# Performance work log

Measured on AMD Instinct MI355X. Metric: run time of the kernel, lower is better.

## Reference

```python
import jax, jax.numpy as jnp
import numpy as np

B, N, C = 4, 2048, 1024
H = 16
D = C // H  # head_dim = 64
NEG = -1e9


def setup_inputs() -> dict:
    key = jax.random.key(0)
    k1, k2, k3, k4 = jax.random.split(key, 4)
    x = jax.random.normal(k1, (B, N, C), dtype=jnp.float32)
    # additive causal mask [N, N]: 0 on/below diagonal, -1e9 above
    causal = jnp.tril(jnp.ones((N, N), dtype=bool))
    attn_mask = jnp.where(causal, 0.0, NEG).astype(jnp.float32)
    # params: qkv Dense (no bias, qkv_bias=False), proj Dense (with bias)
    W_qkv = jax.random.normal(k2, (C, 3 * C), dtype=jnp.float32) / np.sqrt(C)
    W_proj = jax.random.normal(k3, (C, C), dtype=jnp.float32) / np.sqrt(C)
    b_proj = jnp.zeros((C,), dtype=jnp.float32)
    return {"x": x, "attn_mask": attn_mask, "W_qkv": W_qkv,
            "W_proj": W_proj, "b_proj": b_proj}


def reference(x, attn_mask, W_qkv, W_proj, b_proj):
    b, n, c = x.shape
    # qkv projection -> [B, N, 3, H, D] -> q,k,v each [B, H, N, D]
    qkv = (x @ W_qkv).reshape(b, n, 3, H, D)
    qkv = jnp.transpose(qkv, (2, 0, 3, 1, 4))
    q, k, v = qkv[0], qkv[1], qkv[2]
    # unfused attention: full [B, H, N, N] score matrix
    scores = jnp.einsum('bhnd,bhmd->bhnm', q, k) / np.sqrt(D).astype(jnp.float32)
    scores = scores + attn_mask  # broadcast [N, N] over batch/heads
    attn_w = jax.nn.softmax(scores.astype(jnp.float32), axis=-1).astype(scores.dtype)
    out = jnp.einsum('bhnm,bhmd->bhnd', attn_w, v)
    out = jnp.transpose(out, (0, 2, 1, 3)).reshape(b, n, c)
    return out @ W_proj + b_proj
```

## Files before the change

kernel.cpp:

```cpp
#include <hip/hip_runtime.h>
#include <stdint.h>


typedef short s16x8 __attribute__((ext_vector_type(8)));
typedef float f32x4 __attribute__((ext_vector_type(4)));
typedef int i32x2 __attribute__((ext_vector_type(2)));
typedef unsigned int u32;

__device__ __forceinline__ uint16_t f2bf(float f) {
  union { float f; uint32_t u; } v; v.f = f;
  uint32_t r = v.u + 0x7fffu + ((v.u >> 16) & 1u);
  return (uint16_t)(r >> 16);
}

__device__ __forceinline__ u32 cvt_pk_bf16(float lo, float hi) {
  u32 r;
  asm("v_cvt_pk_bf16_f32 %0, %1, %2" : "=v"(r) : "v"(lo), "v"(hi));
  return r;
}

__device__ __forceinline__ s16x8 pack4(u32 w0, u32 w1, u32 w2, u32 w3) {
  union { u32 u[4]; s16x8 v; } t;
  t.u[0] = w0; t.u[1] = w1; t.u[2] = w2; t.u[3] = w3;
  return t.v;
}

#define GLOAD_LDS16(g, l)                                            \
  __builtin_amdgcn_global_load_lds(                                  \
      (const __attribute__((address_space(1))) void*)(g),            \
      (__attribute__((address_space(3))) void*)(l), 16, 0, 0)

__device__ __forceinline__ void transpose32_body(
    const float* __restrict__ src, uint16_t* __restrict__ dst,
    int R, int C, int bx32, int by32, uint16_t (*tile)[33], int tid) {
  const int tx = tid & 31, ty = tid >> 5;
#pragma unroll
  for (int i = 0; i < 32; i += 8)
    tile[ty + i][tx] = f2bf(src[(size_t)(by32 + ty + i) * C + bx32 + tx]);
  __syncthreads();
#pragma unroll
  for (int i = 0; i < 32; i += 8)
    dst[(size_t)(bx32 + ty + i) * R + by32 + tx] = tile[tx][ty + i];
}

__global__ __launch_bounds__(256) void prep_kernel(
    const float* __restrict__ x, uint16_t* __restrict__ xbf,
    const float* __restrict__ Wqkv, uint16_t* __restrict__ wqkvT,
    const float* __restrict__ Wproj, uint16_t* __restrict__ wprojT) {
  __shared__ uint16_t tile[32][33];
  const int bid = blockIdx.x;
  if (bid < 4096) {
    const int i = bid * 256 + threadIdx.x;
    const f32x4 a = ((const f32x4*)x)[2 * i];
    const f32x4 b = ((const f32x4*)x)[2 * i + 1];
    s16x8 r;
    r[0] = (short)f2bf(a[0]); r[1] = (short)f2bf(a[1]);
    r[2] = (short)f2bf(a[2]); r[3] = (short)f2bf(a[3]);
    r[4] = (short)f2bf(b[0]); r[5] = (short)f2bf(b[1]);
    r[6] = (short)f2bf(b[2]); r[7] = (short)f2bf(b[3]);
    ((s16x8*)xbf)[i] = r;
  } else if (bid < 4096 + 3072) {
    const int t = bid - 4096;
    transpose32_body(Wqkv, wqkvT, 1024, 3072, (t % 96) * 32, (t / 96) * 32,
                     tile, threadIdx.x);
  } else {
    const int t = bid - 7168;
    transpose32_body(Wproj, wprojT, 1024, 1024, (t & 31) * 32, (t >> 5) * 32,
                     tile, threadIdx.x);
  }
}

__global__ __launch_bounds__(256) void vtrans_kernel(
    const uint16_t* __restrict__ src, uint16_t* __restrict__ dst) {
  const int bh = blockIdx.y >> 1, dhalf = blockIdx.y & 1;
  const int n0 = blockIdx.x * 32, d0 = dhalf * 32;
  const uint16_t* sb = src + (size_t)bh * 131072;
  uint16_t* db = dst + (size_t)bh * 131072;
  __shared__ uint16_t tile[32][33];
  const int tx = threadIdx.x & 31, ty = threadIdx.x >> 5;
#pragma unroll
  for (int i = 0; i < 32; i += 8)
    tile[ty + i][tx] = sb[(size_t)(n0 + ty + i) * 64 + d0 + tx];
  __syncthreads();
#pragma unroll
  for (int i = 0; i < 32; i += 8)
    db[(size_t)(d0 + ty + i) * 2048 + n0 + tx] = tile[tx][ty + i];
}

template <bool ROUTE>
__global__ __launch_bounds__(256) void gemm_bt_kernel(
    const uint16_t* __restrict__ A, const uint16_t* __restrict__ Bt,
    float* __restrict__ Cout,
    uint16_t* __restrict__ rq, uint16_t* __restrict__ rk, uint16_t* __restrict__ rv,
    const float* __restrict__ bias, int M, int N, int K) {
  __shared__ uint16_t sA[128 * 32];
  __shared__ uint16_t sB[128 * 32];
  const int tid = threadIdx.x;
  const int lane = tid & 63, w = tid >> 6;
  const int l15 = lane & 15, quad = lane >> 4;
  const int row0 = blockIdx.y * 128, col0 = blockIdx.x * 128;
  const int wm = (w >> 1) * 64, wn = (w & 1) * 64;

  f32x4 acc[4][4];
#pragma unroll
  for (int i = 0; i < 4; ++i)
#pragma unroll
    for (int j = 0; j < 4; ++j)
#pragma unroll
      for (int e = 0; e < 4; ++e) acc[i][j][e] = 0.0f;

  for (int k0 = 0; k0 < K; k0 += 32) {
    __syncthreads();
#pragma unroll
    for (int i = 0; i < 2; ++i) {
      const int cbase = i * 256 + w * 64;
      const int c = cbase + lane;
      const int r = c >> 2, kc = (c & 3) * 8;
      GLOAD_LDS16(A + (size_t)(row0 + r) * K + k0 + kc, sA + cbase * 8);
      GLOAD_LDS16(Bt + (size_t)(col0 + r) * K + k0 + kc, sB + cbase * 8);
    }
    __syncthreads();

    s16x8 aF[4], bF[4];
#pragma unroll
    for (int mt = 0; mt < 4; ++mt)
      aF[mt] = *(const s16x8*)(sA + (wm + mt * 16 + l15) * 32 + quad * 8);
#pragma unroll
    for (int nt = 0; nt < 4; ++nt)
      bF[nt] = *(const s16x8*)(sB + (wn + nt * 16 + l15) * 32 + quad * 8);
#pragma unroll
    for (int mt = 0; mt < 4; ++mt)
#pragma unroll
      for (int nt = 0; nt < 4; ++nt)
        acc[mt][nt] = __builtin_amdgcn_mfma_f32_16x16x32_bf16(aF[mt], bF[nt], acc[mt][nt], 0, 0, 0);
  }

  if (ROUTE) {
    const int which = col0 >> 10;
    uint16_t* dst = (which == 0) ? rq : ((which == 1) ? rk : rv);
    const float qs = (which == 0) ? 0.18033688011112042f : 1.0f;
#pragma unroll
    for (int mt = 0; mt < 4; ++mt) {
#pragma unroll
      for (int nt = 0; nt < 4; ++nt) {
        const int colg0 = col0 + wn + nt * 16;
        const int h = (colg0 >> 6) & 15, d0 = colg0 & 63;
#pragma unroll
        for (int i = 0; i < 4; ++i) {
          const int rowg = row0 + wm + mt * 16 + quad * 4 + i;
          const int bh = ((rowg >> 11) << 4) + h, n = rowg & 2047;
          dst[(size_t)bh * 131072 + (size_t)n * 64 + d0 + l15] = f2bf(acc[mt][nt][i] * qs);
        }
      }
    }
  } else {
#pragma unroll
    for (int mt = 0; mt < 4; ++mt) {
#pragma unroll
      for (int nt = 0; nt < 4; ++nt) {
        const int colg = col0 + wn + nt * 16 + l15;
        const float bv = bias[colg];
#pragma unroll
        for (int i = 0; i < 4; ++i) {
          const int rowg = row0 + wm + mt * 16 + quad * 4 + i;
          Cout[(size_t)rowg * N + colg] = acc[mt][nt][i] + bv;
        }
      }
    }
  }
}

__global__ __launch_bounds__(256) void attn_kernel(
    const uint16_t* __restrict__ q_ws, const uint16_t* __restrict__ k_ws,
    const uint16_t* __restrict__ vt_ws, uint16_t* __restrict__ out) {
  const int p = blockIdx.x;
  const int bh = blockIdx.y;
  const int b = bh >> 4, h = bh & 15;
  const int q0L = p * 64, q0H = (31 - p) * 64;
  const int tid = threadIdx.x;
  const int lane = tid & 63, w = tid >> 6;
  const int l15 = lane & 15, quad = lane >> 4;
  const bool qeven = (quad & 1) == 0;

  const uint16_t* qb = q_ws + (size_t)bh * 131072;
  const uint16_t* kb = k_ws + (size_t)bh * 131072;
  const uint16_t* vtb = vt_ws + (size_t)bh * 131072;

  __shared__ uint16_t sK[2][64 * 72];
  __shared__ uint16_t sV[2][64 * 72];

  const int qrowL = q0L + w * 16 + l15;
  const int qrowH = q0H + w * 16 + l15;
  const s16x8 aQL0 = *(const s16x8*)(qb + (size_t)qrowL * 64 + quad * 8);
  const s16x8 aQL1 = *(const s16x8*)(qb + (size_t)qrowL * 64 + 32 + quad * 8);
  const s16x8 aQH0 = *(const s16x8*)(qb + (size_t)qrowH * 64 + quad * 8);
  const s16x8 aQH1 = *(const s16x8*)(qb + (size_t)qrowH * 64 + 32 + quad * 8);

  f32x4 oL[4], oH[4], laccL, laccH;
#pragma unroll
  for (int e = 0; e < 4; ++e) { laccL[e] = 0.0f; laccH[e] = 0.0f; }
#pragma unroll
  for (int i = 0; i < 4; ++i)
#pragma unroll
    for (int e = 0; e < 4; ++e) { oL[i][e] = 0.0f; oH[i][e] = 0.0f; }

  s16x8 bOnes;
#pragma unroll
  for (int j = 0; j < 8; ++j) bOnes[j] = (short)0x3F80;

  const int vr = tid >> 2, dc = (tid & 3) * 16;
  s16x8 rk0 = *(const s16x8*)(kb + (size_t)vr * 64 + dc);
  s16x8 rk1 = *(const s16x8*)(kb + (size_t)vr * 64 + dc + 8);
  s16x8 rv0 = *(const s16x8*)(vtb + (size_t)vr * 2048 + dc);
  s16x8 rv1 = *(const s16x8*)(vtb + (size_t)vr * 2048 + dc + 8);

  const int qrel = w * 16 + l15;

  auto qkt = [&](const s16x8& a0, const s16x8& a1, const uint16_t* sKb,
                 f32x4 (&s)[4]) {
#pragma unroll
    for (int nt = 0; nt < 4; ++nt) {
      f32x4 z;
#pragma unroll
      for (int e = 0; e < 4; ++e) z[e] = 0.0f;
      const s16x8 bK0 = *(const s16x8*)(sKb + (nt * 16 + l15) * 72 + quad * 8);
      const s16x8 bK1 = *(const s16x8*)(sKb + (nt * 16 + l15) * 72 + 32 + quad * 8);
      s[nt] = __builtin_amdgcn_mfma_f32_16x16x32_bf16(bK0, a0, z, 0, 0, 0);
      s[nt] = __builtin_amdgcn_mfma_f32_16x16x32_bf16(bK1, a1, s[nt], 0, 0, 0);
    }
  };

  auto finish = [&](const f32x4 (&s)[4], bool diag, f32x4* o, f32x4& lacc,
                    const uint16_t* sVb) {
#pragma unroll
    for (int kk = 0; kk < 2; ++kk) {
      u32 w0, w1, w2, w3;
#pragma unroll
      for (int t2 = 0; t2 < 2; ++t2) {
        const f32x4& sv = s[2 * kk + t2];
        float pp[4];
        if (diag) {
          const int nt = 2 * kk + t2;
#pragma unroll
          for (int i = 0; i < 4; ++i) {
            const int kv = nt * 16 + quad * 4 + i;
            pp[i] = (kv > qrel) ? 0.0f : __builtin_amdgcn_exp2f(sv[i]);
          }
        } else {
#pragma unroll
          for (int i = 0; i < 4; ++i) pp[i] = __builtin_amdgcn_exp2f(sv[i]);
        }
        const u32 lo = cvt_pk_bf16(pp[0], pp[1]);
        const u32 hi = cvt_pk_bf16(pp[2], pp[3]);
        if (t2 == 0) { w0 = lo; w1 = hi; } else { w2 = lo; w3 = hi; }
      }
      const i32x2 r0 = __builtin_amdgcn_permlane32_swap((int)w0, (int)w2, false, false);
      const i32x2 r1 = __builtin_amdgcn_permlane32_swap((int)w1, (int)w3, false, false);
      const u32 A0 = (u32)r0[0], B0 = (u32)r0[1];
      const u32 A1 = (u32)r1[0], B1 = (u32)r1[1];
      const u32 u0 = qeven ? B0 : A0;
      const u32 u1 = qeven ? B1 : A1;
      const u32 x0 = __shfl_xor(u0, 16);
      const u32 x1 = __shfl_xor(u1, 16);
      const s16x8 aP = pack4(qeven ? A0 : x0, qeven ? A1 : x1,
                             qeven ? x0 : B0, qeven ? x1 : B1);
      lacc = __builtin_amdgcn_mfma_f32_16x16x32_bf16(aP, bOnes, lacc, 0, 0, 0);
#pragma unroll
      for (int dblk = 0; dblk < 4; ++dblk) {
        const s16x8 bV = *(const s16x8*)(sVb + (dblk * 16 + l15) * 72 + kk * 32 + quad * 8);
        o[dblk] = __builtin_amdgcn_mfma_f32_16x16x32_bf16(aP, bV, o[dblk], 0, 0, 0);
      }
    }
  };

  const int TH = q0H >> 6;
  const int TL = q0L >> 6;
  f32x4 sHp[4];

  for (int t = 0; t <= TH; ++t) {
    const int buf = t & 1;
    uint16_t* sKb = sK[buf];
    uint16_t* sVb = sV[buf];
    *(s16x8*)(sKb + vr * 72 + dc) = rk0;
    *(s16x8*)(sKb + vr * 72 + dc + 8) = rk1;
    *(s16x8*)(sVb + vr * 72 + dc) = rv0;
    *(s16x8*)(sVb + vr * 72 + dc + 8) = rv1;
    if (t < TH) {
      const int kvn = (t + 1) << 6;
      rk0 = *(const s16x8*)(kb + (size_t)(kvn + vr) * 64 + dc);
      rk1 = *(const s16x8*)(kb + (size_t)(kvn + vr) * 64 + dc + 8);
      rv0 = *(const s16x8*)(vtb + (size_t)vr * 2048 + kvn + dc);
      rv1 = *(const s16x8*)(vtb + (size_t)vr * 2048 + kvn + dc + 8);
    }
    if (t >= 1) finish(sHp, false, oH, laccH, sV[buf ^ 1]);
    __syncthreads();
    qkt(aQH0, aQH1, sKb, sHp);
    if (t <= TL) {
      f32x4 sLt[4];
      qkt(aQL0, aQL1, sKb, sLt);
      finish(sLt, t == TL, oL, laccL, sVb);
    }
  }
  finish(sHp, true, oH, laccH, sV[TH & 1]);

  const size_t obase = (size_t)b * 2048 * 1024 + (size_t)h * 64;
  auto epi = [&](f32x4* o, const f32x4& lacc, int q0) {
#pragma unroll
    for (int i = 0; i < 4; ++i) {
      const float invi = 1.0f / lacc[i];
      const int row = q0 + w * 16 + quad * 4 + i;
#pragma unroll
      for (int dblk = 0; dblk < 4; ++dblk)
        out[obase + (size_t)row * 1024 + dblk * 16 + l15] = f2bf(o[dblk][i] * invi);
    }
  };
  epi(oH, laccH, q0H);
  epi(oL, laccL, q0L);
}

extern "C" void kernel_launch(void* const* d_in, const int* in_sizes, int n_in,
                              void* d_out, int out_size, void* d_ws, size_t ws_size,
                              hipStream_t stream) {
  (void)in_sizes; (void)n_in; (void)out_size; (void)ws_size;
  const float* x     = (const float*)d_in[0];
  const float* Wqkv  = (const float*)d_in[2];
  const float* Wproj = (const float*)d_in[3];
  const float* bproj = (const float*)d_in[4];
  float* outp = (float*)d_out;

  uint16_t* ws      = (uint16_t*)d_ws;
  uint16_t* q_ws    = ws;
  uint16_t* k_ws    = ws + (size_t)8388608;
  uint16_t* v_ws    = ws + (size_t)16777216;
  uint16_t* attn_ws = ws + (size_t)16777216;
  uint16_t* wqkvT   = ws + (size_t)25165824;
  uint16_t* wprojT  = ws + (size_t)28311552;
  uint16_t* xbf     = (uint16_t*)d_out;
  uint16_t* vt_ws   = (uint16_t*)d_out;

  prep_kernel<<<8192, 256, 0, stream>>>(x, xbf, Wqkv, wqkvT, Wproj, wprojT);
  gemm_bt_kernel<true><<<dim3(24, 64), 256, 0, stream>>>(
      xbf, wqkvT, nullptr, q_ws, k_ws, v_ws, nullptr, 8192, 3072, 1024);
  vtrans_kernel<<<dim3(64, 128), 256, 0, stream>>>(v_ws, vt_ws);
  attn_kernel<<<dim3(16, 64), 256, 0, stream>>>(q_ws, k_ws, vt_ws, attn_ws);
  gemm_bt_kernel<false><<<dim3(8, 64), 256, 0, stream>>>(
      attn_ws, wprojT, outp, nullptr, nullptr, nullptr, bproj, 8192, 1024, 1024);
}
```

Before: 276.6 us.

## Add dedicated double-buffered 256x256 QKV GEMM kernel with swizzled LDS

```diff
diff --git a/kernel.cpp b/kernel.cpp
--- a/kernel.cpp
+++ b/kernel.cpp
@@ -87,12 +87,122 @@
     db[(size_t)(d0 + ty + i) * 2048 + n0 + tx] = tile[tx][ty + i];
 }
 
-template <bool ROUTE>
+__global__ __launch_bounds__(512, 2) void gemm1_kernel(
+    const uint16_t* __restrict__ A, const uint16_t* __restrict__ Bt,
+    uint16_t* __restrict__ rq, uint16_t* __restrict__ rk,
+    uint16_t* __restrict__ rv) {
+  constexpr int K = 1024;
+  constexpr int NT = 16;
+  __shared__ uint16_t sA[2][256 * 64];
+  __shared__ uint16_t sB[2][256 * 64];
+  const int tid = threadIdx.x;
+  const int lane = tid & 63, w = tid >> 6;
+  const int l15 = lane & 15, quad = lane >> 4;
+  const int row0 = blockIdx.y * 256, col0 = blockIdx.x * 256;
+  const int wm = (w >> 2) * 128, wn = (w & 3) * 64;
+
+  const int rA = lane >> 3;
+  const int cXe = ((lane & 7) ^ rA) * 8;
+  const int sgBase = w * 2048;
+
+  const int sx = l15 & 7;
+  const int ok0 = (quad ^ sx) * 8;
+  const int ok1 = ((quad + 4) ^ sx) * 8;
+
+  f32x4 acc[8][4];
+#pragma unroll
+  for (int i = 0; i < 8; ++i)
+#pragma unroll
+    for (int j = 0; j < 4; ++j)
+#pragma unroll
+      for (int e = 0; e < 4; ++e) acc[i][j][e] = 0.0f;
+
+  auto stageA = [&](uint16_t* dst, int kt) {
+#pragma unroll
+    for (int j = 0; j < 4; ++j)
+      GLOAD_LDS16(A + (size_t)(row0 + w * 32 + j * 8 + rA) * K + kt * 64 + cXe,
+                  dst + sgBase + j * 512);
+  };
+  auto stageB = [&](uint16_t* dst, int kt) {
+#pragma unroll
+    for (int j = 0; j < 4; ++j)
+      GLOAD_LDS16(Bt + (size_t)(col0 + w * 32 + j * 8 + rA) * K + kt * 64 + cXe,
+                  dst + sgBase + j * 512);
+  };
+
+  stageA(sA[0], 0);
+  stageB(sB[0], 0);
+
+  int cur = 0;
+  for (int t = 0; t < NT; ++t) {
+    const uint16_t* Ab = sA[cur];
+    const uint16_t* Bb = sB[cur];
+    uint16_t* An = sA[cur ^ 1];
+    uint16_t* Bn = sB[cur ^ 1];
+    const bool haveNext = (t < NT - 1);
+    s16x8 bF[4][2];
+#pragma unroll
+    for (int p = 0; p < 4; ++p) {
+      if (p == 0) {
+        if (haveNext) {
+          stageA(An, t + 1);
+          asm volatile("s_waitcnt vmcnt(4)" ::: "memory");
+        } else {
+          asm volatile("s_waitcnt vmcnt(0)" ::: "memory");
+        }
+        asm volatile("s_barrier" ::: "memory");
+#pragma unroll
+        for (int nt = 0; nt < 4; ++nt) {
+          bF[nt][0] = *(const s16x8*)(Bb + (wn + nt * 16 + l15) * 64 + ok0);
+          bF[nt][1] = *(const s16x8*)(Bb + (wn + nt * 16 + l15) * 64 + ok1);
+        }
+      }
+      if (p == 1 && haveNext) stageB(Bn, t + 1);
+      const int r0 = wm + p * 32 + l15;
+      const s16x8 a00 = *(const s16x8*)(Ab + r0 * 64 + ok0);
+      const s16x8 a01 = *(const s16x8*)(Ab + r0 * 64 + ok1);
+      const s16x8 a10 = *(const s16x8*)(Ab + (r0 + 16) * 64 + ok0);
+      const s16x8 a11 = *(const s16x8*)(Ab + (r0 + 16) * 64 + ok1);
+      __builtin_amdgcn_s_setprio(1);
+#pragma unroll
+      for (int nt = 0; nt < 4; ++nt) {
+        acc[2 * p][nt] =
+            __builtin_amdgcn_mfma_f32_16x16x32_bf16(a00, bF[nt][0], acc[2 * p][nt], 0, 0, 0);
+        acc[2 * p][nt] =
+            __builtin_amdgcn_mfma_f32_16x16x32_bf16(a01, bF[nt][1], acc[2 * p][nt], 0, 0, 0);
+        acc[2 * p + 1][nt] =
+            __builtin_amdgcn_mfma_f32_16x16x32_bf16(a10, bF[nt][0], acc[2 * p + 1][nt], 0, 0, 0);
+        acc[2 * p + 1][nt] =
+            __builtin_amdgcn_mfma_f32_16x16x32_bf16(a11, bF[nt][1], acc[2 * p + 1][nt], 0, 0, 0);
+      }
+      __builtin_amdgcn_s_setprio(0);
+      asm volatile("s_barrier" ::: "memory");
+    }
+    cur ^= 1;
+  }
+
+  const int which = col0 >> 10;
+  uint16_t* dst = (which == 0) ? rq : ((which == 1) ? rk : rv);
+  const float qs = (which == 0) ? 0.18033688011112042f : 1.0f;
+#pragma unroll
+  for (int mt = 0; mt < 8; ++mt) {
+#pragma unroll
+    for (int nt = 0; nt < 4; ++nt) {
+      const int colg0 = col0 + wn + nt * 16;
+      const int h = (colg0 >> 6) & 15, d0 = colg0 & 63;
+#pragma unroll
+      for (int i = 0; i < 4; ++i) {
+        const int rowg = row0 + wm + mt * 16 + quad * 4 + i;
+        const int bh = ((rowg >> 11) << 4) + h, n = rowg & 2047;
+        dst[(size_t)bh * 131072 + (size_t)n * 64 + d0 + l15] = f2bf(acc[mt][nt][i] * qs);
+      }
+    }
+  }
+}
+
 __global__ __launch_bounds__(256) void gemm_bt_kernel(
     const uint16_t* __restrict__ A, const uint16_t* __restrict__ Bt,
-    float* __restrict__ Cout,
-    uint16_t* __restrict__ rq, uint16_t* __restrict__ rk, uint16_t* __restrict__ rv,
-    const float* __restrict__ bias, int M, int N, int K) {
+    float* __restrict__ Cout, const float* __restrict__ bias, int M, int N, int K) {
   __shared__ uint16_t sA[128 * 32];
   __shared__ uint16_t sB[128 * 32];
   const int tid = threadIdx.x;
@@ -135,36 +245,16 @@
         acc[mt][nt] = __builtin_amdgcn_mfma_f32_16x16x32_bf16(aF[mt], bF[nt], acc[mt][nt], 0, 0, 0);
   }
 
-  if (ROUTE) {
-    const int which = col0 >> 10;
-    uint16_t* dst = (which == 0) ? rq : ((which == 1) ? rk : rv);
-    const float qs = (which == 0) ? 0.18033688011112042f : 1.0f;
-#pragma unroll
-    for (int mt = 0; mt < 4; ++mt) {
-#pragma unroll
-      for (int nt = 0; nt < 4; ++nt) {
-        const int colg0 = col0 + wn + nt * 16;
-        const int h = (colg0 >> 6) & 15, d0 = colg0 & 63;
-#pragma unroll
-        for (int i = 0; i < 4; ++i) {
-          const int rowg = row0 + wm + mt * 16 + quad * 4 + i;
-          const int bh = ((rowg >> 11) << 4) + h, n = rowg & 2047;
-          dst[(size_t)bh * 131072 + (size_t)n * 64 + d0 + l15] = f2bf(acc[mt][nt][i] * qs);
-        }
-      }
-    }
-  } else {
-#pragma unroll
-    for (int mt = 0; mt < 4; ++mt) {
-#pragma unroll
-      for (int nt = 0; nt < 4; ++nt) {
-        const int colg = col0 + wn + nt * 16 + l15;
-        const float bv = bias[colg];
-#pragma unroll
-        for (int i = 0; i < 4; ++i) {
-          const int rowg = row0 + wm + mt * 16 + quad * 4 + i;
-          Cout[(size_t)rowg * N + colg] = acc[mt][nt][i] + bv;
-        }
+#pragma unroll
+  for (int mt = 0; mt < 4; ++mt) {
+#pragma unroll
+    for (int nt = 0; nt < 4; ++nt) {
+      const int colg = col0 + wn + nt * 16 + l15;
+      const float bv = bias[colg];
+#pragma unroll
+      for (int i = 0; i < 4; ++i) {
+        const int rowg = row0 + wm + mt * 16 + quad * 4 + i;
+        Cout[(size_t)rowg * N + colg] = acc[mt][nt][i] + bv;
       }
     }
   }
@@ -339,10 +429,9 @@
   uint16_t* vt_ws   = (uint16_t*)d_out;
 
   prep_kernel<<<8192, 256, 0, stream>>>(x, xbf, Wqkv, wqkvT, Wproj, wprojT);
-  gemm_bt_kernel<true><<<dim3(24, 64), 256, 0, stream>>>(
-      xbf, wqkvT, nullptr, q_ws, k_ws, v_ws, nullptr, 8192, 3072, 1024);
+  gemm1_kernel<<<dim3(12, 32), 512, 0, stream>>>(xbf, wqkvT, q_ws, k_ws, v_ws);
   vtrans_kernel<<<dim3(64, 128), 256, 0, stream>>>(v_ws, vt_ws);
   attn_kernel<<<dim3(16, 64), 256, 0, stream>>>(q_ws, k_ws, vt_ws, attn_ws);
-  gemm_bt_kernel<false><<<dim3(8, 64), 256, 0, stream>>>(
-      attn_ws, wprojT, outp, nullptr, nullptr, nullptr, bproj, 8192, 1024, 1024);
-}
+  gemm_bt_kernel<<<dim3(8, 64), 256, 0, stream>>>(
+      attn_ws, wprojT, outp, bproj, 8192, 1024, 1024);
+}
```

Result: slower. 292.4 us (+5.7%).

## Double GEMM K-tile with XOR-swizzled LDS; drop P-operand permlane shuffles in attention

Applied to the files above, without the earlier changes.

```diff
diff --git a/kernel.cpp b/kernel.cpp
--- a/kernel.cpp
+++ b/kernel.cpp
@@ -3,8 +3,8 @@
 
 
 typedef short s16x8 __attribute__((ext_vector_type(8)));
+typedef short s16x4 __attribute__((ext_vector_type(4)));
 typedef float f32x4 __attribute__((ext_vector_type(4)));
-typedef int i32x2 __attribute__((ext_vector_type(2)));
 typedef unsigned int u32;
 
 __device__ __forceinline__ uint16_t f2bf(float f) {
@@ -22,6 +22,12 @@
 __device__ __forceinline__ s16x8 pack4(u32 w0, u32 w1, u32 w2, u32 w3) {
   union { u32 u[4]; s16x8 v; } t;
   t.u[0] = w0; t.u[1] = w1; t.u[2] = w2; t.u[3] = w3;
+  return t.v;
+}
+
+__device__ __forceinline__ s16x8 pack2h(s16x4 a, s16x4 b) {
+  union { s16x4 h[2]; s16x8 v; } t;
+  t.h[0] = a; t.h[1] = b;
   return t.v;
 }
 
@@ -93,8 +99,8 @@
     float* __restrict__ Cout,
     uint16_t* __restrict__ rq, uint16_t* __restrict__ rk, uint16_t* __restrict__ rv,
     const float* __restrict__ bias, int M, int N, int K) {
-  __shared__ uint16_t sA[128 * 32];
-  __shared__ uint16_t sB[128 * 32];
+  __shared__ uint16_t sA[128 * 64];
+  __shared__ uint16_t sB[128 * 64];
   const int tid = threadIdx.x;
   const int lane = tid & 63, w = tid >> 6;
   const int l15 = lane & 15, quad = lane >> 4;
@@ -109,30 +115,37 @@
 #pragma unroll
       for (int e = 0; e < 4; ++e) acc[i][j][e] = 0.0f;
 
-  for (int k0 = 0; k0 < K; k0 += 32) {
+  const int sx = l15 & 7;
+  const int ok[2] = {((0 * 4 + quad) ^ sx) * 8, ((1 * 4 + quad) ^ sx) * 8};
+
+  for (int k0 = 0; k0 < K; k0 += 64) {
     __syncthreads();
 #pragma unroll
-    for (int i = 0; i < 2; ++i) {
+    for (int i = 0; i < 4; ++i) {
       const int cbase = i * 256 + w * 64;
       const int c = cbase + lane;
-      const int r = c >> 2, kc = (c & 3) * 8;
+      const int r = c >> 3;
+      const int kc = ((c & 7) ^ (r & 7)) * 8;
       GLOAD_LDS16(A + (size_t)(row0 + r) * K + k0 + kc, sA + cbase * 8);
       GLOAD_LDS16(Bt + (size_t)(col0 + r) * K + k0 + kc, sB + cbase * 8);
     }
     __syncthreads();
 
-    s16x8 aF[4], bF[4];
-#pragma unroll
-    for (int mt = 0; mt < 4; ++mt)
-      aF[mt] = *(const s16x8*)(sA + (wm + mt * 16 + l15) * 32 + quad * 8);
-#pragma unroll
-    for (int nt = 0; nt < 4; ++nt)
-      bF[nt] = *(const s16x8*)(sB + (wn + nt * 16 + l15) * 32 + quad * 8);
-#pragma unroll
-    for (int mt = 0; mt < 4; ++mt)
+#pragma unroll
+    for (int kk = 0; kk < 2; ++kk) {
+      s16x8 aF[4], bF[4];
+#pragma unroll
+      for (int mt = 0; mt < 4; ++mt)
+        aF[mt] = *(const s16x8*)(sA + (wm + mt * 16 + l15) * 64 + ok[kk]);
 #pragma unroll
       for (int nt = 0; nt < 4; ++nt)
-        acc[mt][nt] = __builtin_amdgcn_mfma_f32_16x16x32_bf16(aF[mt], bF[nt], acc[mt][nt], 0, 0, 0);
+        bF[nt] = *(const s16x8*)(sB + (wn + nt * 16 + l15) * 64 + ok[kk]);
+#pragma unroll
+      for (int mt = 0; mt < 4; ++mt)
+#pragma unroll
+        for (int nt = 0; nt < 4; ++nt)
+          acc[mt][nt] = __builtin_amdgcn_mfma_f32_16x16x32_bf16(aF[mt], bF[nt], acc[mt][nt], 0, 0, 0);
+    }
   }
 
   if (ROUTE) {
@@ -180,7 +193,6 @@
   const int tid = threadIdx.x;
   const int lane = tid & 63, w = tid >> 6;
   const int l15 = lane & 15, quad = lane >> 4;
-  const bool qeven = (quad & 1) == 0;
 
   const uint16_t* qb = q_ws + (size_t)bh * 131072;
   const uint16_t* kb = k_ws + (size_t)bh * 131072;
@@ -234,7 +246,7 @@
                     const uint16_t* sVb) {
 #pragma unroll
     for (int kk = 0; kk < 2; ++kk) {
-      u32 w0, w1, w2, w3;
+      u32 wlo[2], whi[2];
 #pragma unroll
       for (int t2 = 0; t2 < 2; ++t2) {
         const f32x4& sv = s[2 * kk + t2];
@@ -250,24 +262,17 @@
 #pragma unroll
           for (int i = 0; i < 4; ++i) pp[i] = __builtin_amdgcn_exp2f(sv[i]);
         }
-        const u32 lo = cvt_pk_bf16(pp[0], pp[1]);
-        const u32 hi = cvt_pk_bf16(pp[2], pp[3]);
-        if (t2 == 0) { w0 = lo; w1 = hi; } else { w2 = lo; w3 = hi; }
+        wlo[t2] = cvt_pk_bf16(pp[0], pp[1]);
+        whi[t2] = cvt_pk_bf16(pp[2], pp[3]);
       }
-      const i32x2 r0 = __builtin_amdgcn_permlane32_swap((int)w0, (int)w2, false, false);
-      const i32x2 r1 = __builtin_amdgcn_permlane32_swap((int)w1, (int)w3, false, false);
-      const u32 A0 = (u32)r0[0], B0 = (u32)r0[1];
-      const u32 A1 = (u32)r1[0], B1 = (u32)r1[1];
-      const u32 u0 = qeven ? B0 : A0;
-      const u32 u1 = qeven ? B1 : A1;
-      const u32 x0 = __shfl_xor(u0, 16);
-      const u32 x1 = __shfl_xor(u1, 16);
-      const s16x8 aP = pack4(qeven ? A0 : x0, qeven ? A1 : x1,
-                             qeven ? x0 : B0, qeven ? x1 : B1);
+      const s16x8 aP = pack4(wlo[0], whi[0], wlo[1], whi[1]);
       lacc = __builtin_amdgcn_mfma_f32_16x16x32_bf16(aP, bOnes, lacc, 0, 0, 0);
 #pragma unroll
       for (int dblk = 0; dblk < 4; ++dblk) {
-        const s16x8 bV = *(const s16x8*)(sVb + (dblk * 16 + l15) * 72 + kk * 32 + quad * 8);
+        const uint16_t* vrow = sVb + (dblk * 16 + l15) * 72 + kk * 32 + quad * 4;
+        const s16x4 b0 = *(const s16x4*)(vrow);
+        const s16x4 b1 = *(const s16x4*)(vrow + 16);
+        const s16x8 bV = pack2h(b0, b1);
         o[dblk] = __builtin_amdgcn_mfma_f32_16x16x32_bf16(aP, bV, o[dblk], 0, 0, 0);
       }
     }
```

Result: no change. 272.1 us (-1.6%).
